# Optimization experiments

Hardware: AMD Instinct MI355X
Metric: run time of the kernel (lower is better)

The kernel has to match this reference:

```python
import jax, jax.numpy as jnp
import numpy as np
from jax import lax

Z_DIM = 64
ZS_SIZE = [[1, 1]] * 12 + [[2, 1]] + [[2, 2]] * 11 + [[4, 2]] + [[4, 4]] * 11  # 36 embeddings
FILTER = [[16, 16]] * 6 + [[16, 32]] + [[32, 32]] * 5 + [[32, 64]] + [[64, 64]] * 5  # 18 blocks
OFFS = np.cumsum([0] + [h * k for h, k in ZS_SIZE]).tolist()  # 242 z-vectors total


def _hyper(Z, hn_w2, hn_b2, hn_w1, hn_b1):
    # Batched HyperNetwork: Z [n, 64] -> kernels [n, 16, 16, 3, 3]
    n = Z.shape[0]
    h_in = (Z @ hn_w2 + hn_b2).reshape(n, 16, Z_DIM)            # [n, 16, 64]
    h_fin = jnp.einsum('nid,do->nio', h_in, hn_w1) + hn_b1       # [n, 16, 144]
    return h_fin.reshape(n, 16, 16, 3, 3)


def _make_w(z_all, idx, hn_w2, hn_b2, hn_w1, hn_b1):
    # Assemble conv weight [h*16, k*16, 3, 3] from h*k hypernet tiles (cat dim=1 over k, dim=0 over h)
    h, k = ZS_SIZE[idx]
    Z = z_all[OFFS[idx]:OFFS[idx] + h * k]
    K = _hyper(Z, hn_w2, hn_b2, hn_w1, hn_b1)                    # [h*k, 16, 16, 3, 3]
    K = K.reshape(h, k, 16, 16, 3, 3).transpose(0, 2, 1, 3, 4, 5)
    return K.reshape(h * 16, k * 16, 3, 3)


def _conv(x, w, stride, pad):
    return lax.conv_general_dilated(x, w, (stride, stride), [(pad, pad), (pad, pad)],
                                    dimension_numbers=('NCHW', 'OIHW', 'NCHW'))


def _bn(x, i, g, b, m, v):
    # eval-mode BatchNorm2d with running stats; params padded to 64 channels
    C = x.shape[1]
    gg = g[i, :C].reshape(1, C, 1, 1)
    bb = b[i, :C].reshape(1, C, 1, 1)
    mm = m[i, :C].reshape(1, C, 1, 1)
    vv = v[i, :C].reshape(1, C, 1, 1)
    return (x - mm) * (gg * lax.rsqrt(vv + 1e-5)) + bb


def setup_inputs() -> dict:
    key = jax.random.key(0)
    ks = jax.random.split(key, 16)
    B = 1024
    x = jax.random.normal(ks[0], (B, 3, 32, 32), jnp.float32)
    conv1_w = jax.random.normal(ks[1], (16, 3, 3, 3), jnp.float32) / np.float32(np.sqrt(27.0))
    conv1_b = jnp.zeros((16,), jnp.float32)
    n_bn = 37  # bn1 + 2 per block
    bn_gamma = jnp.ones((n_bn, 64), jnp.float32)
    bn_beta = jnp.zeros((n_bn, 64), jnp.float32)
    bn_mean = jnp.zeros((n_bn, 64), jnp.float32)
    bn_var = jnp.ones((n_bn, 64), jnp.float32)
    hn_w2 = jax.random.normal(ks[2], (Z_DIM, 16 * Z_DIM), jnp.float32) * 0.04
    hn_b2 = jax.random.normal(ks[3], (16 * Z_DIM,), jnp.float32) * 0.01
    hn_w1 = jax.random.normal(ks[4], (Z_DIM, 16 * 9), jnp.float32) * 0.04
    hn_b1 = jax.random.normal(ks[5], (16 * 9,), jnp.float32) * 0.01
    z_all = jax.random.normal(ks[6], (OFFS[-1], Z_DIM), jnp.float32)
    res_w6 = jax.random.normal(ks[7], (32, 16, 1, 1), jnp.float32) * 0.25
    res_b6 = jnp.zeros((32,), jnp.float32)
    res_w12 = jax.random.normal(ks[8], (64, 32, 1, 1), jnp.float32) * 0.18
    res_b12 = jnp.zeros((64,), jnp.float32)
    fin_w = jax.random.normal(ks[9], (10, 64), jnp.float32) * 0.1
    fin_b = jnp.zeros((10,), jnp.float32)
    return {"x": x, "conv1_w": conv1_w, "conv1_b": conv1_b,
            "bn_gamma": bn_gamma, "bn_beta": bn_beta, "bn_mean": bn_mean, "bn_var": bn_var,
            "hn_w2": hn_w2, "hn_b2": hn_b2, "hn_w1": hn_w1, "hn_b1": hn_b1,
            "z_all": z_all, "res_w6": res_w6, "res_b6": res_b6,
            "res_w12": res_w12, "res_b12": res_b12, "fin_w": fin_w, "fin_b": fin_b}


def reference(x, conv1_w, conv1_b, bn_gamma, bn_beta, bn_mean, bn_var,
              hn_w2, hn_b2, hn_w1, hn_b1, z_all,
              res_w6, res_b6, res_w12, res_b12, fin_w, fin_b):
    x = _conv(x, conv1_w, 1, 1) + conv1_b.reshape(1, -1, 1, 1)
    x = jax.nn.relu(_bn(x, 0, bn_gamma, bn_beta, bn_mean, bn_var))
    for i in range(18):
        w1 = _make_w(z_all, 2 * i, hn_w2, hn_b2, hn_w1, hn_b1)
        w2 = _make_w(z_all, 2 * i + 1, hn_w2, hn_b2, hn_w1, hn_b1)
        down = (i > 5 and i % 6 == 0)
        if down:
            rw, rb = (res_w6, res_b6) if i == 6 else (res_w12, res_b12)
            res = _conv(x, rw, 2, 0) + rb.reshape(1, -1, 1, 1)
            stride = 2
        else:
            res = x
            stride = 1
        out = jax.nn.relu(_bn(_conv(x, w1, stride, 1), 1 + 2 * i, bn_gamma, bn_beta, bn_mean, bn_var))
        out = _bn(_conv(out, w2, 1, 1), 2 + 2 * i, bn_gamma, bn_beta, bn_mean, bn_var)
        x = jax.nn.relu(out + res)
    x = x.mean(axis=(2, 3))  # AvgPool2d(8) on [B,64,8,8]
    return x @ fin_w.T + fin_b
```

## Files before the change

kernel.cpp:

```cpp
#include <hip/hip_runtime.h>
#include <hip/hip_bf16.h>


typedef __attribute__((ext_vector_type(8))) short bf16x8;
typedef __attribute__((ext_vector_type(4))) float f32x4;
typedef unsigned short ushort_t;

#define OFFS_LIST {0,1,2,3,4,5,6,7,8,9,10,11,12,14,18,22,26,30,34,38,42,46,50,54,58,66,82,98,114,130,146,162,178,194,210,226,242}
#define K_LIST    {1,1,1,1,1,1,1,1,1,1,1,1,1,2,2,2,2,2,2,2,2,2,2,2,2,4,4,4,4,4,4,4,4,4,4,4}
#define H_LIST    {1,1,1,1,1,1,1,1,1,1,1,1,2,2,2,2,2,2,2,2,2,2,2,2,4,4,4,4,4,4,4,4,4,4,4,4}
#define WOFF_LIST {0,2304,4608,6912,9216,11520,13824,16128,18432,20736,23040,25344,27648,32256,41472,50688,59904,69120,78336,87552,96768,105984,115200,124416,133632,152064,188928,225792,262656,299520,336384,373248,410112,446976,483840,520704}
#define CIN_LIST  {16,16,16,16,16,16,16,16,16,16,16,16,16,32,32,32,32,32,32,32,32,32,32,32,32,64,64,64,64,64,64,64,64,64,64,64}
#define COUT_LIST {16,16,16,16,16,16,16,16,16,16,16,16,32,32,32,32,32,32,32,32,32,32,32,32,64,64,64,64,64,64,64,64,64,64,64,64}
#define WFOFF_LIST {0,7680,15360,23040,30720,38400,46080,53760,61440,69120,76800,84480,92160,107520,135168,162816,190464,218112,245760,273408,301056,328704,356352,384000,411648,466944,577536,688128,798720,909312,1019904,1130496,1241088,1351680,1462272,1572864}

__constant__ int d_offs[37]  = OFFS_LIST;
__constant__ int d_k[36]     = K_LIST;
__constant__ int d_hh[36]    = H_LIST;
__constant__ int d_woff[36]  = WOFF_LIST;
__constant__ int d_cin[36]   = CIN_LIST;
__constant__ int d_cout[36]  = COUT_LIST;
__constant__ int d_wfoff[36] = WFOFF_LIST;

__device__ inline void split3(float x, ushort_t& h, ushort_t& m, ushort_t& l) {
    unsigned xb = __float_as_uint(x);
    unsigned hb = (xb + 0x8000u) >> 16;
    float fh = __uint_as_float(hb << 16);
    float r = x - fh;
    unsigned rb2 = __float_as_uint(r);
    unsigned mb = (rb2 + 0x8000u) >> 16;
    float fm = __uint_as_float(mb << 16);
    float r2 = r - fm;
    unsigned lb = (__float_as_uint(r2) + 0x8000u) >> 16;
    h = (ushort_t)hb; m = (ushort_t)mb; l = (ushort_t)lb;
}

__global__ void prep(const float* __restrict__ g, const float* __restrict__ be,
                     const float* __restrict__ m, const float* __restrict__ v,
                     const float* __restrict__ rw6, const float* __restrict__ rw12,
                     float* __restrict__ sc, float* __restrict__ sh,
                     float* __restrict__ rwT6, float* __restrict__ rwT12) {
    int i = blockIdx.x * blockDim.x + threadIdx.x;
    if (i < 2368) {
        float s = g[i] * rsqrtf(v[i] + 1e-5f);
        sc[i] = s;
        sh[i] = be[i] - m[i] * s;
    } else if (i < 2368 + 512) {
        int t = i - 2368;
        int co = t % 32, ci = t / 32;
        rwT6[ci * 32 + co] = rw6[co * 16 + ci];
    } else if (i < 2368 + 512 + 2048) {
        int t = i - 2368 - 512;
        int co = t % 64, ci = t / 64;
        rwT12[ci * 64 + co] = rw12[co * 32 + ci];
    }
}

__global__ void hyper_kernel(const float* __restrict__ z_all, const float* __restrict__ w2,
                             const float* __restrict__ b2, const float* __restrict__ w1,
                             const float* __restrict__ b1, const float* __restrict__ bnsc,
                             float* __restrict__ Wg) {
    int n = blockIdx.x;
    int tid = threadIdx.x;
    __shared__ float zrow[64];
    __shared__ float hin[1024];
    if (tid < 64) zrow[tid] = z_all[n * 64 + tid];
    __syncthreads();
    for (int mcol = tid; mcol < 1024; mcol += 256) {
        float acc = b2[mcol];
        #pragma unroll 8
        for (int d = 0; d < 64; ++d) acc += zrow[d] * w2[d * 1024 + mcol];
        hin[mcol] = acc;
    }
    __syncthreads();
    int L = 0;
    while (n >= d_offs[L + 1]) ++L;
    int r = n - d_offs[L];
    int kk = d_k[L];
    int a = r / kk, bb = r % kk;
    int Cin = kk * 16;
    int Cout = d_hh[L] * 16;
    const float* scp = bnsc + (L + 1) * 64;
    float* wp = Wg + d_woff[L];
    for (int e = tid; e < 2304; e += 256) {
        int i = e / 144, o = e % 144;
        int j = o / 9, tap = o % 9;
        float acc = b1[o];
        #pragma unroll 8
        for (int d = 0; d < 64; ++d) acc += hin[i * 64 + d] * w1[d * 144 + o];
        int co = a * 16 + i;
        acc *= scp[co];
        wp[(tap * Cin + (bb * 16 + j)) * Cout + co] = acc;
    }
}

__global__ void split_w(const float* __restrict__ Wg, ushort_t* __restrict__ Wf) {
    int L = blockIdx.y;
    int CIN = d_cin[L], COUT = d_cout[L];
    int K = 9 * CIN, NKS = (K + 31) / 32, NT = COUT / 16;
    int total = NKS * NT * 512;
    int idx = blockIdx.x * 256 + threadIdx.x;
    if (idx >= total) return;
    int j = idx & 7, lane = (idx >> 3) & 63, t = idx >> 9;
    int nt = t % NT, ks = t / NT;
    int gg = lane >> 4, r16 = lane & 15;
    int k = ks * 32 + gg * 8 + j, co = nt * 16 + r16;
    float wv = (k < K) ? Wg[d_woff[L] + k * COUT + co] : 0.f;
    ushort_t h, m, l;
    split3(wv, h, m, l);
    int base = d_wfoff[L] + ((ks * NT + nt) * 3) * 512 + lane * 8 + j;
    Wf[base] = h; Wf[base + 512] = m; Wf[base + 1024] = l;
}

__global__ void conv_first(const float* __restrict__ x, const float* __restrict__ cw,
                           const float* __restrict__ cb, const float* __restrict__ g,
                           const float* __restrict__ be, const float* __restrict__ m,
                           const float* __restrict__ v, float* __restrict__ out) {
    int idx = blockIdx.x * 256 + threadIdx.x;
    int px = idx & 31; int t = idx >> 5;
    int py = t & 31;   int b = t >> 5;
    float acc[16];
    #pragma unroll
    for (int co = 0; co < 16; ++co) acc[co] = 0.f;
    const float* ip = x + (long)b * 3 * 1024;
    #pragma unroll 1
    for (int ci = 0; ci < 3; ++ci) {
        #pragma unroll 1
        for (int ky = 0; ky < 3; ++ky) {
            int iy = py + ky - 1;
            if ((unsigned)iy >= 32u) continue;
            #pragma unroll
            for (int kx = 0; kx < 3; ++kx) {
                int ix = px + kx - 1;
                if ((unsigned)ix < 32u) {
                    float xv = ip[ci * 1024 + iy * 32 + ix];
                    #pragma unroll
                    for (int co = 0; co < 16; ++co)
                        acc[co] += xv * cw[co * 27 + ci * 9 + ky * 3 + kx];
                }
            }
        }
    }
    long o = ((long)(b * 32 + py) * 32 + px) * 16;
    #pragma unroll
    for (int co = 0; co < 16; ++co) {
        float s = g[co] * rsqrtf(v[co] + 1e-5f);
        float val = (acc[co] + cb[co] - m[co]) * s + be[co];
        out[o + co] = fmaxf(val, 0.f);
    }
}

template<int CIN, int COUT, int HIN, int STRIDE, int TH, int TW, int MODE, int CR, int HR>
__global__ __launch_bounds__(256) void conv_mfma(
        const float* __restrict__ in, const ushort_t* __restrict__ wf,
        const float* __restrict__ shp, const float* __restrict__ res,
        const float* __restrict__ rwT, const float* __restrict__ rb,
        float* __restrict__ out) {
    constexpr int HOUT = HIN / STRIDE;
    constexpr int CG8 = CIN / 8;
    constexpr int IH = (TH - 1) * STRIDE + 3;
    constexpr int IW = (TW - 1) * STRIDE + 3;
    constexpr int K = 9 * CIN;
    constexpr int NKS = (K + 31) / 32;
    constexpr bool TAIL = (K % 32) != 0;
    constexpr int NT = COUT / 16;
    constexpr int NMT = TH * TW / 16;
    constexpr int MTW = NMT / 4;
    constexpr int PADC = ((2 - (IH * IW)) % 8 + 8) % 8;
    constexpr int CSTU = IH * IW + PADC;
    constexpr int PST = CG8 * CSTU;
    constexpr int TX = HOUT / TW, TY = HOUT / TH;

    __shared__ uint4 lds[3 * PST];

    int tid = threadIdx.x;
    int bid = blockIdx.x;
    int tile = bid % (TY * TX);
    int b = bid / (TY * TX);
    int ty = tile / TX, tx = tile % TX;
    int Y0 = ty * TH, X0 = tx * TW;
    int gy0 = Y0 * STRIDE - 1, gx0 = X0 * STRIDE - 1;

    for (int e = tid; e < CG8 * IH * IW; e += 256) {
        int c8 = e / (IH * IW); int rr = e % (IH * IW);
        int ly = rr / IW, lx = rr % IW;
        int gy = gy0 + ly, gx = gx0 + lx;
        float vv[8];
        if ((unsigned)gy < (unsigned)HIN && (unsigned)gx < (unsigned)HIN) {
            const float4* p = (const float4*)(in + ((long)(b * HIN + gy) * HIN + gx) * CIN + c8 * 8);
            float4 a0 = p[0], a1 = p[1];
            vv[0]=a0.x; vv[1]=a0.y; vv[2]=a0.z; vv[3]=a0.w;
            vv[4]=a1.x; vv[5]=a1.y; vv[6]=a1.z; vv[7]=a1.w;
        } else {
            #pragma unroll
            for (int q = 0; q < 8; ++q) vv[q] = 0.f;
        }
        union { ushort_t u[8]; uint4 q4; } H, M, L;
        #pragma unroll
        for (int q = 0; q < 8; ++q) split3(vv[q], H.u[q], M.u[q], L.u[q]);
        int a16 = c8 * CSTU + rr;
        lds[a16] = H.q4; lds[PST + a16] = M.q4; lds[2 * PST + a16] = L.q4;
    }
    __syncthreads();

    int lane = tid & 63, wid = tid >> 6;
    int g = lane >> 4, r16 = lane & 15;

    f32x4 acc[MTW][NT] = {};

    int pbase[MTW];
    #pragma unroll
    for (int mt = 0; mt < MTW; ++mt) {
        int pid = (wid + 4 * mt) * 16 + r16;
        int py = pid / TW, px = pid % TW;
        pbase[mt] = (py * STRIDE) * IW + px * STRIDE;
    }

    #pragma unroll
    for (int ks = 0; ks < NKS; ++ks) {
        bf16x8 bfr[NT][3];
        #pragma unroll
        for (int nt = 0; nt < NT; ++nt)
            #pragma unroll
            for (int p = 0; p < 3; ++p)
                bfr[nt][p] = *(const bf16x8*)(wf + ((ks * NT + nt) * 3 + p) * 512 + lane * 8);

        int k0 = ks * 32 + g * 8;
        int tap = k0 / CIN;
        int ci8 = (k0 % CIN) >> 3;
        int ky = (tap * 11) >> 5;
        int kx = tap - 3 * ky;
        int ofs = ci8 * CSTU + ky * IW + kx;

        #pragma unroll
        for (int mt = 0; mt < MTW; ++mt) {
            int e16 = ofs + pbase[mt];
            if (TAIL && ks == NKS - 1) e16 = (g < 2) ? e16 : 0;
            const uint4* ap = lds + e16;
            bf16x8 ah = *(const bf16x8*)(ap);
            bf16x8 am = *(const bf16x8*)(ap + PST);
            bf16x8 al = *(const bf16x8*)(ap + 2 * PST);
            #pragma unroll
            for (int nt = 0; nt < NT; ++nt) {
                f32x4 c = acc[mt][nt];
                c = __builtin_amdgcn_mfma_f32_16x16x32_bf16(ah, bfr[nt][0], c, 0, 0, 0);
                c = __builtin_amdgcn_mfma_f32_16x16x32_bf16(ah, bfr[nt][1], c, 0, 0, 0);
                c = __builtin_amdgcn_mfma_f32_16x16x32_bf16(am, bfr[nt][0], c, 0, 0, 0);
                c = __builtin_amdgcn_mfma_f32_16x16x32_bf16(ah, bfr[nt][2], c, 0, 0, 0);
                c = __builtin_amdgcn_mfma_f32_16x16x32_bf16(am, bfr[nt][1], c, 0, 0, 0);
                c = __builtin_amdgcn_mfma_f32_16x16x32_bf16(al, bfr[nt][0], c, 0, 0, 0);
                acc[mt][nt] = c;
            }
        }
    }

    #pragma unroll
    for (int mt = 0; mt < MTW; ++mt) {
        #pragma unroll
        for (int nt = 0; nt < NT; ++nt) {
            int co = nt * 16 + r16;
            float shv = shp[co];
            #pragma unroll
            for (int reg = 0; reg < 4; ++reg) {
                int pid = (wid + 4 * mt) * 16 + g * 4 + reg;
                int py = pid / TW, px = pid % TW;
                int gy = Y0 + py, gx = X0 + px;
                long oidx = ((long)(b * HOUT + gy) * HOUT + gx) * COUT + co;
                float val = acc[mt][nt][reg] + shv;
                if (MODE == 1) val += res[oidx];
                if (MODE == 2) {
                    float racc = rb[co];
                    const float* rp = res + ((long)(b * HR + 2 * gy) * HR + 2 * gx) * CR;
                    #pragma unroll 4
                    for (int ci = 0; ci < CR; ++ci) racc += rp[ci] * rwT[ci * COUT + co];
                    val += racc;
                }
                out[oidx] = fmaxf(val, 0.f);
            }
        }
    }
}

__global__ void pool_fc(const float* __restrict__ X, const float* __restrict__ fw,
                        const float* __restrict__ fb, float* __restrict__ out) {
    int b = blockIdx.x;
    int c = threadIdx.x;
    float s = 0.f;
    #pragma unroll
    for (int p = 0; p < 64; ++p) s += X[((long)b * 64 + p) * 64 + c];
    __shared__ float pooled[64];
    pooled[c] = s * (1.f / 64.f);
    __syncthreads();
    if (c < 10) {
        float acc = fb[c];
        #pragma unroll
        for (int k = 0; k < 64; ++k) acc += pooled[k] * fw[c * 64 + k];
        out[b * 10 + c] = acc;
    }
}

extern "C" void kernel_launch(void* const* d_in, const int* in_sizes, int n_in,
                              void* d_out, int out_size, void* d_ws, size_t ws_size,
                              hipStream_t stream) {
    const float* x       = (const float*)d_in[0];
    const float* conv1_w = (const float*)d_in[1];
    const float* conv1_b = (const float*)d_in[2];
    const float* bn_g    = (const float*)d_in[3];
    const float* bn_b    = (const float*)d_in[4];
    const float* bn_m    = (const float*)d_in[5];
    const float* bn_v    = (const float*)d_in[6];
    const float* hn_w2   = (const float*)d_in[7];
    const float* hn_b2   = (const float*)d_in[8];
    const float* hn_w1   = (const float*)d_in[9];
    const float* hn_b1   = (const float*)d_in[10];
    const float* z_all   = (const float*)d_in[11];
    const float* res_w6  = (const float*)d_in[12];
    const float* res_b6  = (const float*)d_in[13];
    const float* res_w12 = (const float*)d_in[14];
    const float* res_b12 = (const float*)d_in[15];
    const float* fin_w   = (const float*)d_in[16];
    const float* fin_b   = (const float*)d_in[17];
    float* outp = (float*)d_out;

    float* wsf      = (float*)d_ws;
    float* Wg       = wsf;
    float* bnsc     = wsf + 557568;
    float* bnsh     = wsf + 559936;
    float* rwT6     = wsf + 562304;
    float* rwT12    = wsf + 562816;
    ushort_t* Wfrag = (ushort_t*)(wsf + 564864);
    float* act0     = wsf + (1 << 21);
    float* act1     = act0 + (1 << 24);
    float* act2     = act1 + (1 << 24);

    static const int woff[36]  = WOFF_LIST;
    static const int wfoff[36] = WFOFF_LIST;
    (void)woff;

    prep<<<20, 256, 0, stream>>>(bn_g, bn_b, bn_m, bn_v, res_w6, res_w12,
                                 bnsc, bnsh, rwT6, rwT12);
    hyper_kernel<<<242, 256, 0, stream>>>(z_all, hn_w2, hn_b2, hn_w1, hn_b1, bnsc, Wg);
    split_w<<<dim3(144, 36), 256, 0, stream>>>(Wg, Wfrag);
    conv_first<<<4096, 256, 0, stream>>>(x, conv1_w, conv1_b, bn_g, bn_b, bn_m, bn_v, act0);

    float* X = act0; float* T1 = act1; float* T2 = act2;
    for (int i = 0; i < 18; ++i) {
        int L1 = 2 * i, L2 = 2 * i + 1;
        const ushort_t* w1p = Wfrag + wfoff[L1];
        const ushort_t* w2p = Wfrag + wfoff[L2];
        const float* s1p = bnsh + (L1 + 1) * 64;
        const float* s2p = bnsh + (L2 + 1) * 64;
        if (i < 6) {
            conv_mfma<16,16,32,1,16,16,0,1,1><<<4096, 256, 0, stream>>>(
                X, w1p, s1p, nullptr, nullptr, nullptr, T1);
            conv_mfma<16,16,32,1,16,16,1,1,1><<<4096, 256, 0, stream>>>(
                T1, w2p, s2p, X, nullptr, nullptr, T2);
        } else if (i == 6) {
            conv_mfma<16,32,32,2,8,16,0,1,1><<<2048, 256, 0, stream>>>(
                X, w1p, s1p, nullptr, nullptr, nullptr, T1);
            conv_mfma<32,32,16,1,8,16,2,16,32><<<2048, 256, 0, stream>>>(
                T1, w2p, s2p, X, rwT6, res_b6, T2);
        } else if (i < 12) {
            conv_mfma<32,32,16,1,8,16,0,1,1><<<2048, 256, 0, stream>>>(
                X, w1p, s1p, nullptr, nullptr, nullptr, T1);
            conv_mfma<32,32,16,1,8,16,1,1,1><<<2048, 256, 0, stream>>>(
                T1, w2p, s2p, X, nullptr, nullptr, T2);
        } else if (i == 12) {
            conv_mfma<32,64,16,2,8,8,0,1,1><<<1024, 256, 0, stream>>>(
                X, w1p, s1p, nullptr, nullptr, nullptr, T1);
            conv_mfma<64,64,8,1,8,8,2,32,16><<<1024, 256, 0, stream>>>(
                T1, w2p, s2p, X, rwT12, res_b12, T2);
        } else {
            conv_mfma<64,64,8,1,8,8,0,1,1><<<1024, 256, 0, stream>>>(
                X, w1p, s1p, nullptr, nullptr, nullptr, T1);
            conv_mfma<64,64,8,1,8,8,1,1,1><<<1024, 256, 0, stream>>>(
                T1, w2p, s2p, X, nullptr, nullptr, T2);
        }
        float* tmp = X; X = T2; T2 = tmp;
    }
    pool_fc<<<1024, 64, 0, stream>>>(X, fin_w, fin_b, outp);
}
```

Measured before the change: 1.354 ms.

## Add 32x32 MFMA conv path with padded pre-split bf16x3 activation layout

For stages 2 and 3 (32- and 64-channel layers), activations are stored as spatially padded NHWC buffers already split into three bf16 parts. A new conv_mx kernel reads its MFMA operands straight from global memory, with no LDS staging, and uses 32x32x16 MFMAs plus a double-buffered load/compute loop. The stride-2 residual 1x1 conv of block 12 is folded into the main GEMM as extra K-steps, with its bias merged into the BN shift. This removes LDS tiling and fp32-to-bf16 splitting of inputs on every layer, at the cost of more global traffic per thread, extra pad_zero launches, and a more complex weight packing.

```diff
diff --git a/kernel.cpp b/kernel.cpp
--- a/kernel.cpp
+++ b/kernel.cpp
@@ -4,6 +4,7 @@
 
 typedef __attribute__((ext_vector_type(8))) short bf16x8;
 typedef __attribute__((ext_vector_type(4))) float f32x4;
+typedef __attribute__((ext_vector_type(16))) float f32x16;
 typedef unsigned short ushort_t;
 
 #define OFFS_LIST {0,1,2,3,4,5,6,7,8,9,10,11,12,14,18,22,26,30,34,38,42,46,50,54,58,66,82,98,114,130,146,162,178,194,210,226,242}
@@ -12,7 +13,7 @@
 #define WOFF_LIST {0,2304,4608,6912,9216,11520,13824,16128,18432,20736,23040,25344,27648,32256,41472,50688,59904,69120,78336,87552,96768,105984,115200,124416,133632,152064,188928,225792,262656,299520,336384,373248,410112,446976,483840,520704}
 #define CIN_LIST  {16,16,16,16,16,16,16,16,16,16,16,16,16,32,32,32,32,32,32,32,32,32,32,32,32,64,64,64,64,64,64,64,64,64,64,64}
 #define COUT_LIST {16,16,16,16,16,16,16,16,16,16,16,16,32,32,32,32,32,32,32,32,32,32,32,32,64,64,64,64,64,64,64,64,64,64,64,64}
-#define WFOFF_LIST {0,7680,15360,23040,30720,38400,46080,53760,61440,69120,76800,84480,92160,107520,135168,162816,190464,218112,245760,273408,301056,328704,356352,384000,411648,466944,577536,688128,798720,909312,1019904,1130496,1241088,1351680,1462272,1572864}
+#define WFOFF_LIST {0,7680,15360,23040,30720,38400,46080,53760,61440,69120,76800,84480,92160,107520,135168,165888,196608,227328,258048,288768,319488,350208,380928,411648,442368,503808,632832,755712,878592,1001472,1124352,1247232,1370112,1492992,1615872,1738752}
 
 __constant__ int d_offs[37]  = OFFS_LIST;
 __constant__ int d_k[36]     = K_LIST;
@@ -27,19 +28,19 @@
     unsigned hb = (xb + 0x8000u) >> 16;
     float fh = __uint_as_float(hb << 16);
     float r = x - fh;
-    unsigned rb2 = __float_as_uint(r);
-    unsigned mb = (rb2 + 0x8000u) >> 16;
+    unsigned mb = (__float_as_uint(r) + 0x8000u) >> 16;
     float fm = __uint_as_float(mb << 16);
     float r2 = r - fm;
     unsigned lb = (__float_as_uint(r2) + 0x8000u) >> 16;
     h = (ushort_t)hb; m = (ushort_t)mb; l = (ushort_t)lb;
 }
+__device__ inline float b2f(ushort_t u) { return __uint_as_float(((unsigned)u) << 16); }
 
 __global__ void prep(const float* __restrict__ g, const float* __restrict__ be,
                      const float* __restrict__ m, const float* __restrict__ v,
-                     const float* __restrict__ rw6, const float* __restrict__ rw12,
+                     const float* __restrict__ rw6, const float* __restrict__ rb12,
                      float* __restrict__ sc, float* __restrict__ sh,
-                     float* __restrict__ rwT6, float* __restrict__ rwT12) {
+                     float* __restrict__ rwT6, float* __restrict__ shp25) {
     int i = blockIdx.x * blockDim.x + threadIdx.x;
     if (i < 2368) {
         float s = g[i] * rsqrtf(v[i] + 1e-5f);
@@ -49,10 +50,11 @@
         int t = i - 2368;
         int co = t % 32, ci = t / 32;
         rwT6[ci * 32 + co] = rw6[co * 16 + ci];
-    } else if (i < 2368 + 512 + 2048) {
-        int t = i - 2368 - 512;
-        int co = t % 64, ci = t / 64;
-        rwT12[ci * 64 + co] = rw12[co * 32 + ci];
+    } else if (i < 2368 + 512 + 64) {
+        int c = i - 2880;
+        int idx2 = 26 * 64 + c;
+        float s = g[idx2] * rsqrtf(v[idx2] + 1e-5f);
+        shp25[c] = be[idx2] - m[idx2] * s + rb12[c];
     }
 }
 
@@ -94,21 +96,41 @@
     }
 }
 
-__global__ void split_w(const float* __restrict__ Wg, ushort_t* __restrict__ Wf) {
+__global__ void split_w(const float* __restrict__ Wg, const float* __restrict__ rw12,
+                        ushort_t* __restrict__ Wf) {
     int L = blockIdx.y;
     int CIN = d_cin[L], COUT = d_cout[L];
-    int K = 9 * CIN, NKS = (K + 31) / 32, NT = COUT / 16;
-    int total = NKS * NT * 512;
     int idx = blockIdx.x * 256 + threadIdx.x;
-    if (idx >= total) return;
     int j = idx & 7, lane = (idx >> 3) & 63, t = idx >> 9;
-    int nt = t % NT, ks = t / NT;
-    int gg = lane >> 4, r16 = lane & 15;
-    int k = ks * 32 + gg * 8 + j, co = nt * 16 + r16;
-    float wv = (k < K) ? Wg[d_woff[L] + k * COUT + co] : 0.f;
+    int hi = lane >> 5;
+    float wv;
+    int base;
+    if (L < 14) {
+        int K = 9 * CIN, NKS = (K + 31) / 32, NT = COUT / 16;
+        if (t >= NKS * NT) return;
+        int nt = t % NT, ks = t / NT;
+        int k = ks * 32 + (lane >> 4) * 8 + j;
+        int co = nt * 16 + (lane & 15);
+        wv = (k < K) ? Wg[d_woff[L] + k * COUT + co] : 0.f;
+        base = d_wfoff[L] + ((ks * NT + nt) * 3) * 512 + lane * 8 + j;
+    } else {
+        int CG8 = CIN / 8, NKS = 5 * CG8, NT = COUT / 32;
+        int TKS = NKS + ((L == 25) ? 2 : 0);
+        if (t >= TKS * NT) return;
+        int nt = t % NT, ks = t / NT;
+        int co = nt * 32 + (lane & 31);
+        if (ks < NKS) {
+            int o = 2 * ks + hi, tap = o % 10, c8 = o / 10;
+            int ci = c8 * 8 + j;
+            wv = (tap < 9) ? Wg[d_woff[L] + (tap * CIN + ci) * COUT + co] : 0.f;
+        } else {
+            int k = (ks - NKS) * 16 + hi * 8 + j;
+            wv = rw12[co * 32 + k];
+        }
+        base = d_wfoff[L] + ((ks * NT + nt) * 3) * 512 + lane * 8 + j;
+    }
     ushort_t h, m, l;
     split3(wv, h, m, l);
-    int base = d_wfoff[L] + ((ks * NT + nt) * 3) * 512 + lane * 8 + j;
     Wf[base] = h; Wf[base + 512] = m; Wf[base + 1024] = l;
 }
 
@@ -150,12 +172,28 @@
     }
 }
 
-template<int CIN, int COUT, int HIN, int STRIDE, int TH, int TW, int MODE, int CR, int HR>
+__global__ void pad_zero(ushort_t* __restrict__ buf, int H2, int pxc ) {
+    int idx = blockIdx.x * 256 + threadIdx.x;
+    int nb = 2 * H2 + 2 * (H2 - 2);
+    int total = 1024 * nb * pxc;
+    if (idx >= total) return;
+    int ch = idx % pxc; int t = idx / pxc;
+    int bp = t % nb; int img = t / nb;
+    int y, x;
+    if (bp < H2) { y = 0; x = bp; }
+    else if (bp < 2 * H2) { y = H2 - 1; x = bp - H2; }
+    else { int s = bp - 2 * H2; y = 1 + (s >> 1); x = (s & 1) ? H2 - 1 : 0; }
+    long off = ((long)img * H2 * H2 + y * H2 + x) * (pxc * 8) + ch * 8;
+    uint4 z = make_uint4(0, 0, 0, 0);
+    *(uint4*)(buf + off) = z;
+}
+
+template<int CIN, int COUT, int HIN, int STRIDE, int TH, int TW, int MODE, int CR, int HR, int OUTF>
 __global__ __launch_bounds__(256) void conv_mfma(
         const float* __restrict__ in, const ushort_t* __restrict__ wf,
         const float* __restrict__ shp, const float* __restrict__ res,
         const float* __restrict__ rwT, const float* __restrict__ rb,
-        float* __restrict__ out) {
+        float* __restrict__ out, ushort_t* __restrict__ outp2) {
     constexpr int HOUT = HIN / STRIDE;
     constexpr int CG8 = CIN / 8;
     constexpr int IH = (TH - 1) * STRIDE + 3;
@@ -265,9 +303,11 @@
                 int pid = (wid + 4 * mt) * 16 + g * 4 + reg;
                 int py = pid / TW, px = pid % TW;
                 int gy = Y0 + py, gx = X0 + px;
-                long oidx = ((long)(b * HOUT + gy) * HOUT + gx) * COUT + co;
                 float val = acc[mt][nt][reg] + shv;
-                if (MODE == 1) val += res[oidx];
+                if (MODE == 1) {
+                    long oidx = ((long)(b * HOUT + gy) * HOUT + gx) * COUT + co;
+                    val += res[oidx];
+                }
                 if (MODE == 2) {
                     float racc = rb[co];
                     const float* rp = res + ((long)(b * HR + 2 * gy) * HR + 2 * gx) * CR;
@@ -275,19 +315,145 @@
                     for (int ci = 0; ci < CR; ++ci) racc += rp[ci] * rwT[ci * COUT + co];
                     val += racc;
                 }
-                out[oidx] = fmaxf(val, 0.f);
+                val = fmaxf(val, 0.f);
+                if (OUTF == 0) {
+                    long oidx = ((long)(b * HOUT + gy) * HOUT + gx) * COUT + co;
+                    out[oidx] = val;
+                } else {
+                    ushort_t* pp = outp2 + (long)b * 31104
+                                   + ((gy + 1) * 18 + gx + 1) * 96 + (co >> 3) * 24 + (co & 7);
+                    ushort_t h, m2, l;
+                    split3(val, h, m2, l);
+                    pp[0] = h; pp[8] = m2; pp[16] = l;
+                }
             }
         }
     }
 }
 
-__global__ void pool_fc(const float* __restrict__ X, const float* __restrict__ fw,
+template<int CIN, int COUT, int HIN, int STRIDE, int MODE, int RKS, int RH2, int RPXI>
+__global__ __launch_bounds__(256) void conv_mx(
+        const ushort_t* __restrict__ in, const ushort_t* __restrict__ wf,
+        const float* __restrict__ shp, const ushort_t* __restrict__ res,
+        ushort_t* __restrict__ out) {
+    constexpr int CG8 = CIN / 8;
+    constexpr int NKS = 5 * CG8;
+    constexpr int TKS = NKS + RKS;
+    constexpr int HOUT = HIN / STRIDE, H2I = HIN + 2, H2O = HOUT + 2;
+    constexpr int PXI = CIN * 3, PXO = COUT * 3;
+    constexpr long IMGI = (long)H2I * H2I * PXI, IMGO = (long)H2O * H2O * PXO;
+    constexpr int NT = COUT / 32, MT = HOUT * HOUT / 32;
+
+    int tid = threadIdx.x, lane = tid & 63, wid = tid >> 6;
+    int wg = blockIdx.x * 4 + wid;
+    int img = wg / MT, mt = wg % MT;
+    int lp = lane & 31, hi = lane >> 5;
+    int pix = mt * 32 + lp;
+    int py = pix / HOUT, px = pix % HOUT;
+
+    const ushort_t* abase = in + (long)img * IMGI + ((py * STRIDE) * H2I + px * STRIDE) * PXI;
+    const ushort_t* rbase = (RKS > 0)
+        ? res + (long)img * ((long)RH2 * RH2 * RPXI) + ((2 * py + 1) * RH2 + (2 * px + 1)) * RPXI
+        : nullptr;
+    const ushort_t* wfl = wf + lane * 8;
+
+    f32x16 acc[NT] = {};
+
+    auto LK = [&](int ks, bf16x8 (&x)[3], bf16x8 (&w)[NT][3]) {
+        const ushort_t* ap;
+        if (RKS > 0 && ks >= NKS) {
+            int c8 = 2 * (ks - NKS) + hi;
+            ap = rbase + c8 * 24;
+        } else {
+            int o = 2 * ks + hi;
+            int tap = o % 10, c8 = o / 10;
+            int ky = (tap * 11) >> 5, kx = tap - 3 * ky;
+            int aofs = (ky * H2I + kx) * PXI + c8 * 24;
+            if (tap == 9) aofs = 0;
+            ap = abase + aofs;
+        }
+        x[0] = *(const bf16x8*)(ap);
+        x[1] = *(const bf16x8*)(ap + 8);
+        x[2] = *(const bf16x8*)(ap + 16);
+        #pragma unroll
+        for (int nt = 0; nt < NT; ++nt)
+            #pragma unroll
+            for (int p = 0; p < 3; ++p)
+                w[nt][p] = *(const bf16x8*)(wfl + ((ks * NT + nt) * 3 + p) * 512);
+    };
+    auto DO = [&](bf16x8 (&x)[3], bf16x8 (&w)[NT][3]) {
+        #pragma unroll
+        for (int nt = 0; nt < NT; ++nt) {
+            f32x16 c = acc[nt];
+            c = __builtin_amdgcn_mfma_f32_32x32x16_bf16(w[nt][0], x[0], c, 0, 0, 0);
+            c = __builtin_amdgcn_mfma_f32_32x32x16_bf16(w[nt][1], x[0], c, 0, 0, 0);
+            c = __builtin_amdgcn_mfma_f32_32x32x16_bf16(w[nt][0], x[1], c, 0, 0, 0);
+            c = __builtin_amdgcn_mfma_f32_32x32x16_bf16(w[nt][2], x[0], c, 0, 0, 0);
+            c = __builtin_amdgcn_mfma_f32_32x32x16_bf16(w[nt][1], x[1], c, 0, 0, 0);
+            c = __builtin_amdgcn_mfma_f32_32x32x16_bf16(w[nt][0], x[2], c, 0, 0, 0);
+            acc[nt] = c;
+        }
+    };
+
+    bf16x8 xA[3], wA[NT][3], xB[3], wB[NT][3];
+    LK(0, xA, wA);
+    #pragma unroll
+    for (int ks = 0; ks < TKS; ks += 2) {
+        LK(ks + 1, xB, wB);
+        DO(xA, wA);
+        if (ks + 2 < TKS) LK(ks + 2, xA, wA);
+        DO(xB, wB);
+    }
+
+    ushort_t* ob = out + (long)img * IMGO + ((py + 1) * H2O + (px + 1)) * PXO;
+    const ushort_t* rs = (MODE == 1)
+        ? res + (long)img * IMGO + ((py + 1) * H2O + (px + 1)) * PXO : nullptr;
+    #pragma unroll
+    for (int nt = 0; nt < NT; ++nt) {
+        #pragma unroll
+        for (int q = 0; q < 4; ++q) {
+            int cob = nt * 32 + q * 8 + 4 * hi;
+            float v[4];
+            #pragma unroll
+            for (int t = 0; t < 4; ++t) v[t] = acc[nt][4 * q + t] + shp[cob + t];
+            if (MODE == 1) {
+                const ushort_t* rp = rs + (nt * 4 + q) * 24 + 4 * hi;
+                ushort4 rh = *(const ushort4*)(rp);
+                ushort4 rm = *(const ushort4*)(rp + 8);
+                ushort4 rl = *(const ushort4*)(rp + 16);
+                v[0] += b2f(rh.x) + b2f(rm.x) + b2f(rl.x);
+                v[1] += b2f(rh.y) + b2f(rm.y) + b2f(rl.y);
+                v[2] += b2f(rh.z) + b2f(rm.z) + b2f(rl.z);
+                v[3] += b2f(rh.w) + b2f(rm.w) + b2f(rl.w);
+            }
+            ushort4 h4, m4, l4;
+            #pragma unroll
+            for (int t = 0; t < 4; ++t) {
+                float val = fmaxf(v[t], 0.f);
+                ushort_t h, m2, l;
+                split3(val, h, m2, l);
+                ((ushort_t*)&h4)[t] = h; ((ushort_t*)&m4)[t] = m2; ((ushort_t*)&l4)[t] = l;
+            }
+            ushort_t* pp = ob + (nt * 4 + q) * 24 + 4 * hi;
+            *(ushort4*)(pp) = h4;
+            *(ushort4*)(pp + 8) = m4;
+            *(ushort4*)(pp + 16) = l4;
+        }
+    }
+}
+
+__global__ void pool_fc(const ushort_t* __restrict__ X, const float* __restrict__ fw,
                         const float* __restrict__ fb, float* __restrict__ out) {
     int b = blockIdx.x;
     int c = threadIdx.x;
+    const ushort_t* ib = X + (long)b * 19200 + (c >> 3) * 24 + (c & 7);
     float s = 0.f;
     #pragma unroll
-    for (int p = 0; p < 64; ++p) s += X[((long)b * 64 + p) * 64 + c];
+    for (int p = 0; p < 64; ++p) {
+        int y = p >> 3, x = p & 7;
+        int base = ((y + 1) * 10 + (x + 1)) * 192;
+        s += b2f(ib[base]) + b2f(ib[base + 8]) + b2f(ib[base + 16]);
+    }
     __shared__ float pooled[64];
     pooled[c] = s * (1.f / 64.f);
     __syncthreads();
@@ -327,56 +493,66 @@
     float* bnsc     = wsf + 557568;
     float* bnsh     = wsf + 559936;
     float* rwT6     = wsf + 562304;
-    float* rwT12    = wsf + 562816;
-    ushort_t* Wfrag = (ushort_t*)(wsf + 564864);
-    float* act0     = wsf + (1 << 21);
-    float* act1     = act0 + (1 << 24);
-    float* act2     = act1 + (1 << 24);
-
-    static const int woff[36]  = WOFF_LIST;
+    float* shp25    = wsf + 564864;
+    ushort_t* Wfrag = (ushort_t*)(wsf + 565248);
+
+    float*    A0f = (float*)((char*)d_ws + (size_t)(16) * (1 << 20));
+    float*    A1f = (float*)((char*)d_ws + (size_t)(80) * (1 << 20));
+    float*    A2f = (float*)((char*)d_ws + (size_t)(144) * (1 << 20));
+    ushort_t* A0s = (ushort_t*)A0f;
+    ushort_t* A1s = (ushort_t*)A1f;
+    ushort_t* A2s = (ushort_t*)A2f;
+
     static const int wfoff[36] = WFOFF_LIST;
-    (void)woff;
-
-    prep<<<20, 256, 0, stream>>>(bn_g, bn_b, bn_m, bn_v, res_w6, res_w12,
-                                 bnsc, bnsh, rwT6, rwT12);
+
+    prep<<<20, 256, 0, stream>>>(bn_g, bn_b, bn_m, bn_v, res_w6, res_b12,
+                                 bnsc, bnsh, rwT6, shp25);
     hyper_kernel<<<242, 256, 0, stream>>>(z_all, hn_w2, hn_b2, hn_w1, hn_b1, bnsc, Wg);
-    split_w<<<dim3(144, 36), 256, 0, stream>>>(Wg, Wfrag);
-    conv_first<<<4096, 256, 0, stream>>>(x, conv1_w, conv1_b, bn_g, bn_b, bn_m, bn_v, act0);
-
-    float* X = act0; float* T1 = act1; float* T2 = act2;
-    for (int i = 0; i < 18; ++i) {
+    split_w<<<dim3(168, 36), 256, 0, stream>>>(Wg, res_w12, Wfrag);
+    conv_first<<<4096, 256, 0, stream>>>(x, conv1_w, conv1_b, bn_g, bn_b, bn_m, bn_v, A0f);
+
+    float* X = A0f; float* T1 = A1f; float* T2 = A2f;
+    for (int i = 0; i < 6; ++i) {
         int L1 = 2 * i, L2 = 2 * i + 1;
-        const ushort_t* w1p = Wfrag + wfoff[L1];
-        const ushort_t* w2p = Wfrag + wfoff[L2];
-        const float* s1p = bnsh + (L1 + 1) * 64;
-        const float* s2p = bnsh + (L2 + 1) * 64;
-        if (i < 6) {
-            conv_mfma<16,16,32,1,16,16,0,1,1><<<4096, 256, 0, stream>>>(
-                X, w1p, s1p, nullptr, nullptr, nullptr, T1);
-            conv_mfma<16,16,32,1,16,16,1,1,1><<<4096, 256, 0, stream>>>(
-                T1, w2p, s2p, X, nullptr, nullptr, T2);
-        } else if (i == 6) {
-            conv_mfma<16,32,32,2,8,16,0,1,1><<<2048, 256, 0, stream>>>(
-                X, w1p, s1p, nullptr, nullptr, nullptr, T1);
-            conv_mfma<32,32,16,1,8,16,2,16,32><<<2048, 256, 0, stream>>>(
-                T1, w2p, s2p, X, rwT6, res_b6, T2);
-        } else if (i < 12) {
-            conv_mfma<32,32,16,1,8,16,0,1,1><<<2048, 256, 0, stream>>>(
-                X, w1p, s1p, nullptr, nullptr, nullptr, T1);
-            conv_mfma<32,32,16,1,8,16,1,1,1><<<2048, 256, 0, stream>>>(
-                T1, w2p, s2p, X, nullptr, nullptr, T2);
-        } else if (i == 12) {
-            conv_mfma<32,64,16,2,8,8,0,1,1><<<1024, 256, 0, stream>>>(
-                X, w1p, s1p, nullptr, nullptr, nullptr, T1);
-            conv_mfma<64,64,8,1,8,8,2,32,16><<<1024, 256, 0, stream>>>(
-                T1, w2p, s2p, X, rwT12, res_b12, T2);
-        } else {
-            conv_mfma<64,64,8,1,8,8,0,1,1><<<1024, 256, 0, stream>>>(
-                X, w1p, s1p, nullptr, nullptr, nullptr, T1);
-            conv_mfma<64,64,8,1,8,8,1,1,1><<<1024, 256, 0, stream>>>(
-                T1, w2p, s2p, X, nullptr, nullptr, T2);
-        }
+        conv_mfma<16,16,32,1,16,16,0,1,1,0><<<4096, 256, 0, stream>>>(
+            X, Wfrag + wfoff[L1], bnsh + (L1 + 1) * 64, nullptr, nullptr, nullptr, T1, nullptr);
+        conv_mfma<16,16,32,1,16,16,1,1,1,0><<<4096, 256, 0, stream>>>(
+            T1, Wfrag + wfoff[L2], bnsh + (L2 + 1) * 64, X, nullptr, nullptr, T2, nullptr);
         float* tmp = X; X = T2; T2 = tmp;
     }
-    pool_fc<<<1024, 64, 0, stream>>>(X, fin_w, fin_b, outp);
-}
+    conv_mfma<16,32,32,2,8,16,0,1,1,0><<<2048, 256, 0, stream>>>(
+        A0f, Wfrag + wfoff[12], bnsh + 13 * 64, nullptr, nullptr, nullptr, A1f, nullptr);
+    pad_zero<<<3264, 256, 0, stream>>>(A2s, 18, 12);
+    conv_mfma<32,32,16,1,8,16,2,16,32,1><<<2048, 256, 0, stream>>>(
+        A1f, Wfrag + wfoff[13], bnsh + 14 * 64, A0f, rwT6, res_b6, nullptr, A2s);
+    pad_zero<<<3264, 256, 0, stream>>>(A1s, 18, 12);
+    pad_zero<<<3264, 256, 0, stream>>>(A0s, 18, 12);
+
+    ushort_t* Xs = A2s; ushort_t* T1s = A1s; ushort_t* T2s = A0s;
+    for (int i = 7; i < 12; ++i) {
+        int L1 = 2 * i, L2 = 2 * i + 1;
+        conv_mx<32,32,16,1,0,0,1,1><<<2048, 256, 0, stream>>>(
+            Xs, Wfrag + wfoff[L1], bnsh + (L1 + 1) * 64, nullptr, T1s);
+        conv_mx<32,32,16,1,1,0,1,1><<<2048, 256, 0, stream>>>(
+            T1s, Wfrag + wfoff[L2], bnsh + (L2 + 1) * 64, Xs, T2s);
+        ushort_t* tmp = Xs; Xs = T2s; T2s = tmp;
+    }
+    pad_zero<<<3456, 256, 0, stream>>>(A1s, 10, 24);
+    pad_zero<<<3456, 256, 0, stream>>>(A2s, 10, 24);
+    conv_mx<32,64,16,2,0,0,1,1><<<512, 256, 0, stream>>>(
+        A0s, Wfrag + wfoff[24], bnsh + 25 * 64, nullptr, A1s);
+    conv_mx<64,64,8,1,0,2,18,96><<<512, 256, 0, stream>>>(
+        A1s, Wfrag + wfoff[25], shp25, A0s, A2s);
+    pad_zero<<<3456, 256, 0, stream>>>(A0s, 10, 24);
+
+    Xs = A2s; T1s = A1s; T2s = A0s;
+    for (int i = 13; i < 18; ++i) {
+        int L1 = 2 * i, L2 = 2 * i + 1;
+        conv_mx<64,64,8,1,0,0,1,1><<<512, 256, 0, stream>>>(
+            Xs, Wfrag + wfoff[L1], bnsh + (L1 + 1) * 64, nullptr, T1s);
+        conv_mx<64,64,8,1,1,0,1,1><<<512, 256, 0, stream>>>(
+            T1s, Wfrag + wfoff[L2], bnsh + (L2 + 1) * 64, Xs, T2s);
+        ushort_t* tmp = Xs; Xs = T2s; T2s = tmp;
+    }
+    pool_fc<<<1024, 64, 0, stream>>>(Xs, fin_w, fin_b, outp);
+}
```

New measurement: 2.241 ms. 65.4% more time.
